# Optimization experiments

Measured on AMD Instinct MI355X. Metric: run time of the kernel, lower is better.

Reference implementation:

```python
import jax, jax.numpy as jnp
import numpy as np

B, T, D, E, H, K = 4, 4096, 1024, 8, 512, 2  # batch, seq, n_embed, num_experts, bottleneck, top_k


def setup_inputs() -> dict:
    key = jax.random.key(0)
    ks = jax.random.split(key, 8)
    s = 0.02  # param scale (original zero-inits adapters; random used for a meaningful baseline)
    return {
        "x": jax.random.normal(ks[0], (B, T, D), jnp.float32),
        "Wr": (jax.random.normal(ks[1], (D, E), jnp.float32) * s),
        "br": jnp.zeros((E,), jnp.float32),
        "Wn": (jax.random.normal(ks[2], (D, E), jnp.float32) * s),
        "bn": jnp.zeros((E,), jnp.float32),
        "Wd": (jax.random.normal(ks[3], (E, D, H), jnp.float32) * s),
        "bd": jnp.zeros((E, H), jnp.float32),
        "Wu": (jax.random.normal(ks[4], (E, H, D), jnp.float32) * s),
        "bu": jnp.zeros((E, D), jnp.float32),
        "noise": jax.random.normal(ks[5], (B, T, E), jnp.float32),
        "top_k": K,
    }


def reference(x, Wr, br, Wn, bn, Wd, bd, Wu, bu, noise, top_k):
    # --- NoisyTopkRouter ---
    logits = x @ Wr + br                                   # [B,T,E]
    noise_logits = x @ Wn + bn                             # [B,T,E]
    noisy = logits + noise * jax.nn.softplus(noise_logits)  # randn * softplus(noise_logits)
    _, idx = jax.lax.top_k(noisy, top_k)                   # [B,T,K]
    # mask of selected experts; where(mask, noisy, -inf) == scatter(top_k_logits into -inf)
    mask = jax.nn.one_hot(idx, noisy.shape[-1], dtype=jnp.bool_).any(axis=-2)  # [B,T,E]
    sparse = jnp.where(mask, noisy, -jnp.inf)
    gates = jax.nn.softmax(sparse, axis=-1)                # zeros for unselected experts

    # --- Experts (dense grouped form; gate==0 exactly kills unselected experts incl. biases) ---
    down = jnp.einsum('btd,edh->bteh', x, Wd) + bd         # [B,T,E,H]
    hidden = jax.nn.gelu(down, approximate=False)          # torch GELU is exact (erf)
    up = jnp.einsum('bteh,ehd->bted', hidden, Wu) + bu     # [B,T,E,D]
    return jnp.einsum('bted,bte->btd', up, gates)          # gate-weighted combine
```

## Files before the change

### kernel.cpp

```cpp
#include <hip/hip_runtime.h>
#include <hip/hip_bf16.h>
#include <hip/hip_fp16.h>
#include <math.h>

#define DD   1024
#define EE   8
#define HH   512
#define NTOK 16384
#define NG   16
#define MAXMT 24
#define NT   (NG * MAXMT)

typedef __attribute__((ext_vector_type(8))) short short8;
typedef __attribute__((ext_vector_type(4))) float floatx4;

__device__ __forceinline__ ushort f2bfu(float f) {
    __hip_bfloat16 h = __float2bfloat16(f);
    return *reinterpret_cast<ushort*>(&h);
}
__device__ __forceinline__ float bfu2f(ushort u) {
    union { unsigned u; float f; } cv; cv.u = ((unsigned)u) << 16; return cv.f;
}

__device__ __forceinline__ void glds16(const void* g, void* l) {
    __builtin_amdgcn_global_load_lds(
        (const __attribute__((address_space(1))) unsigned int*)g,
        (__attribute__((address_space(3))) unsigned int*)l, 16, 0, 0);
}

__global__ __launch_bounds__(256) void trans_k(const float* __restrict__ src, ushort* __restrict__ dst,
                                               const int R, const int C, int* __restrict__ cnt) {
    if (cnt && blockIdx.x == 0 && blockIdx.y == 0 && blockIdx.z == 0 && threadIdx.x < 256)
        cnt[threadIdx.x] = 0;
    const int e = blockIdx.z, r0 = blockIdx.y * 64, c0 = blockIdx.x * 64;
    __shared__ float t[64][65];
    const int tid = threadIdx.x;
    const int cseg = (tid & 15) * 4, rr = tid >> 4;
#pragma unroll
    for (int j = 0; j < 4; ++j) {
        const int r = rr + j * 16;
        const float4 v = *(const float4*)(src + ((size_t)e * R + r0 + r) * C + c0 + cseg);
        t[r][cseg] = v.x; t[r][cseg+1] = v.y; t[r][cseg+2] = v.z; t[r][cseg+3] = v.w;
    }
    __syncthreads();
    const int rseg = (tid & 15) * 4;
#pragma unroll
    for (int j = 0; j < 4; ++j) {
        const int crow = (tid >> 4) + j * 16;
        ushort o[4];
#pragma unroll
        for (int q = 0; q < 4; ++q) o[q] = f2bfu(t[rseg + q][crow]);
        *(uint2*)(dst + ((size_t)e * C + c0 + crow) * R + r0 + rseg) = *(uint2*)o;
    }
}

#define ROUTER_TAIL(AR, AN, T) do {                                           \
    const int t_ = (T);                                                       \
    float noisy[EE];                                                          \
    _Pragma("unroll")                                                         \
    for (int e = 0; e < EE; ++e) {                                            \
        const float lg = AR[e] + br[e];                                       \
        const float nl = AN[e] + bn[e];                                       \
        const float sp = fmaxf(nl, 0.f) + log1pf(expf(-fabsf(nl)));           \
        noisy[e] = lg + noise[(size_t)t_ * EE + e] * sp;                      \
    }                                                                         \
    int i0 = 0;                                                               \
    _Pragma("unroll")                                                         \
    for (int e = 1; e < EE; ++e) if (noisy[e] > noisy[i0]) i0 = e;            \
    int i1 = (i0 == 0) ? 1 : 0;                                               \
    _Pragma("unroll")                                                         \
    for (int e = 0; e < EE; ++e) if (e != i0 && noisy[e] > noisy[i1]) i1 = e; \
    const float ex = expf(noisy[i1] - noisy[i0]);                             \
    const float g0 = 1.f / (1.f + ex);                                        \
    const float g1 = ex / (1.f + ex);                                         \
    __half h0 = __float2half_rn(g0), h1 = __float2half_rn(g1);                \
    const unsigned u0 = (unsigned)t_ | ((unsigned)*reinterpret_cast<ushort*>(&h0) << 16); \
    const unsigned u1 = (unsigned)t_ | ((unsigned)*reinterpret_cast<ushort*>(&h1) << 16); \
    const int ga = i0 * 2 + 0, gb = i1 * 2 + 1;                               \
    int p0 = atomicAdd(&cnt[ga * 16], 1);                                     \
    entries[ga * NTOK + p0] = u0;                                             \
    int p1 = atomicAdd(&cnt[gb * 16], 1);                                     \
    entries[gb * NTOK + p1] = u1;                                             \
} while (0)

__global__ __launch_bounds__(512) void router_k(
    const float* __restrict__ x, const float* __restrict__ Wr, const float* __restrict__ br,
    const float* __restrict__ Wn, const float* __restrict__ bn, const float* __restrict__ noise,
    int* __restrict__ cnt, unsigned* __restrict__ entries, ushort* __restrict__ xb)
{
    __shared__ __align__(16) float WT[DD * 20];

    const int tid = threadIdx.x;
    {
        const int d0 = tid * 2;
#pragma unroll
        for (int r = 0; r < 2; ++r) {
            const int d = d0 + r;
            float4 a = *(const float4*)(Wr + (size_t)d * EE);
            float4 b = *(const float4*)(Wr + (size_t)d * EE + 4);
            float4 c = *(const float4*)(Wn + (size_t)d * EE);
            float4 e4 = *(const float4*)(Wn + (size_t)d * EE + 4);
            float* row = &WT[d * 20];
            *(float4*)(row + 0)  = a;
            *(float4*)(row + 4)  = b;
            *(float4*)(row + 8)  = c;
            *(float4*)(row + 12) = e4;
        }
    }
    __syncthreads();

    const int wave = tid >> 6;
    const int lane = tid & 63;
    const int t0 = blockIdx.x * 16 + wave * 2;

    float a0r[EE], a0n[EE], a1r[EE], a1n[EE];
#pragma unroll
    for (int e = 0; e < EE; ++e) { a0r[e] = 0.f; a0n[e] = 0.f; a1r[e] = 0.f; a1n[e] = 0.f; }

    const float* xr0 = x + (size_t)t0 * DD;
    const float* xr1 = xr0 + DD;
    ushort* xb0 = xb + (size_t)t0 * DD;
    ushort* xb1 = xb0 + DD;

#pragma unroll 4
    for (int s = 0; s < DD / 64; ++s) {
        const int d = s * 64 + lane;
        const float x0 = xr0[d];
        const float x1 = xr1[d];
        xb0[d] = f2bfu(x0);
        xb1[d] = f2bfu(x1);
        const float* row = &WT[d * 20];
        const float4 w0 = *(const float4*)(row + 0);
        const float4 w1 = *(const float4*)(row + 4);
        const float4 w2 = *(const float4*)(row + 8);
        const float4 w3 = *(const float4*)(row + 12);
        const float wr[8] = { w0.x, w0.y, w0.z, w0.w, w1.x, w1.y, w1.z, w1.w };
        const float wn[8] = { w2.x, w2.y, w2.z, w2.w, w3.x, w3.y, w3.z, w3.w };
#pragma unroll
        for (int e = 0; e < EE; ++e) {
            a0r[e] = fmaf(x0, wr[e], a0r[e]);
            a0n[e] = fmaf(x0, wn[e], a0n[e]);
            a1r[e] = fmaf(x1, wr[e], a1r[e]);
            a1n[e] = fmaf(x1, wn[e], a1n[e]);
        }
    }
#pragma unroll
    for (int off = 32; off > 0; off >>= 1) {
#pragma unroll
        for (int e = 0; e < EE; ++e) {
            a0r[e] += __shfl_xor(a0r[e], off);
            a0n[e] += __shfl_xor(a0n[e], off);
            a1r[e] += __shfl_xor(a1r[e], off);
            a1n[e] += __shfl_xor(a1n[e], off);
        }
    }
    if (lane == 0) {
        ROUTER_TAIL(a0r, a0n, t0);
        ROUTER_TAIL(a1r, a1n, t0 + 1);
    }
}


__global__ __launch_bounds__(256) void down_k(
    const ushort* __restrict__ xb, const ushort* __restrict__ WdT, const float* __restrict__ bd,
    const int* __restrict__ cnt, const unsigned* __restrict__ entries, ushort* __restrict__ hid)
{
    const int bx = blockIdx.x;
    const int n0 = (bx / NT) * 128;
    const int tmg = bx % NT;
    const int tm = tmg % MAXMT;
    const int g = tmg / MAXMT, e = g >> 1;
    const int n_g = cnt[g * 16];
    if (tm * 128 >= n_g) return;

    int og = 0;
    for (int gg = 0; gg < g; ++gg) og += cnt[gg * 16];

    __shared__ __align__(16) ushort As[2 * 128 * 64];
    __shared__ __align__(16) ushort Bs[2 * 128 * 64];
    __shared__ unsigned ecache[128];

    const int tid = threadIdx.x, lane = tid & 63, w = tid >> 6;
    const int wm = w >> 1, wn = w & 1;
    const int fr = lane & 15, fq = lane >> 4;

    if (tid < 128) {
        const int ridx = min(tm * 128 + tid, n_g - 1);
        ecache[tid] = entries[g * NTOK + ridx];
    }
    __syncthreads();

    const int lr = lane >> 3, seg = lane & 7;
    const int slog = seg ^ lr;
    const ushort* gA[4]; const ushort* gB[4];
    int loff[4];
    const ushort* WTe = WdT + (size_t)e * HH * DD;
#pragma unroll
    for (int j = 0; j < 4; ++j) {
        const int row = w * 32 + j * 8 + lr;
        const int tok = (int)(ecache[row] & 0xFFFFu);
        gA[j] = xb + (size_t)tok * DD + slog * 8;
        gB[j] = WTe + (size_t)(n0 + row) * DD + slog * 8;
        loff[j] = (w * 256 + j * 64) * 16;
    }

    floatx4 acc[4][4];
#pragma unroll
    for (int i = 0; i < 4; ++i)
#pragma unroll
        for (int j = 0; j < 4; ++j) acc[i][j] = (floatx4){0.f, 0.f, 0.f, 0.f};

    const int axr = wm * 64 + fr;
    const int bxr = wn * 64 + fr;

#pragma unroll
    for (int j = 0; j < 4; ++j) {
        glds16(gA[j], (char*)As + loff[j]);
        glds16(gB[j], (char*)Bs + loff[j]);
    }
    __syncthreads();

    int cur = 0;
    for (int k0 = 0; k0 < DD; k0 += 64) {
        if (k0 + 64 < DD) {
            const int nb = (cur ^ 1) * 16384;
#pragma unroll
            for (int j = 0; j < 4; ++j) {
                glds16(gA[j] + k0 + 64, (char*)As + nb + loff[j]);
                glds16(gB[j] + k0 + 64, (char*)Bs + nb + loff[j]);
            }
        }
        const int cb = cur * 8192;
#pragma unroll
        for (int kh = 0; kh < 2; ++kh) {
            short8 a[4], b[4];
#pragma unroll
            for (int mt = 0; mt < 4; ++mt) {
                const int r = axr + mt * 16;
                a[mt] = *(const short8*)&As[cb + r * 64 + ((kh * 4 + fq) ^ (r & 7)) * 8];
            }
#pragma unroll
            for (int nt = 0; nt < 4; ++nt) {
                const int r = bxr + nt * 16;
                b[nt] = *(const short8*)&Bs[cb + r * 64 + ((kh * 4 + fq) ^ (r & 7)) * 8];
            }
#pragma unroll
            for (int mt = 0; mt < 4; ++mt)
#pragma unroll
                for (int nt = 0; nt < 4; ++nt)
                    acc[mt][nt] = __builtin_amdgcn_mfma_f32_16x16x32_bf16(a[mt], b[nt], acc[mt][nt], 0, 0, 0);
        }
        __syncthreads();
        cur ^= 1;
    }

    const int hbase = og + tm * 128;
#pragma unroll
    for (int nt = 0; nt < 4; ++nt) {
        const int n = n0 + wn * 64 + nt * 16 + fr;
        const float bias = bd[e * HH + n];
#pragma unroll
        for (int mt = 0; mt < 4; ++mt)
#pragma unroll
            for (int i = 0; i < 4; ++i) {
                const int rl = wm * 64 + mt * 16 + fq * 4 + i;
                if (tm * 128 + rl < n_g) {
                    const float v = acc[mt][nt][i] + bias;
                    const float ge = 0.5f * v * (1.f + erff(v * 0.7071067811865475f));
                    hid[(size_t)(hbase + rl) * HH + n] = f2bfu(ge);
                }
            }
    }
}

__global__ __launch_bounds__(256) void up_k(
    const ushort* __restrict__ hid, const ushort* __restrict__ WuT, const float* __restrict__ bu,
    const int* __restrict__ cnt, const unsigned* __restrict__ entries, ushort* __restrict__ slots)
{
    const int bx = blockIdx.x;
    const int n0 = (bx / NT) * 128;
    const int tmg = bx % NT;
    const int tm = tmg % MAXMT;
    const int g = tmg / MAXMT, e = g >> 1, slot = g & 1;
    const int n_g = cnt[g * 16];
    if (tm * 128 >= n_g) return;

    int hbase = 0;
    for (int gg = 0; gg < g; ++gg) hbase += cnt[gg * 16];

    __shared__ __align__(16) ushort As[2 * 128 * 64];
    __shared__ __align__(16) ushort Bs[2 * 128 * 64];
    __shared__ unsigned ecache[128];

    const int tid = threadIdx.x, lane = tid & 63, w = tid >> 6;
    const int wm = w >> 1, wn = w & 1;
    const int fr = lane & 15, fq = lane >> 4;

    if (tid < 128) {
        const int ridx = min(tm * 128 + tid, n_g - 1);
        ecache[tid] = entries[g * NTOK + ridx];
    }
    __syncthreads();

    const int lr = lane >> 3, seg = lane & 7;
    const int slog = seg ^ lr;
    const ushort* gA[4]; const ushort* gB[4];
    int loff[4];
    const ushort* WTe = WuT + (size_t)e * DD * HH;
#pragma unroll
    for (int j = 0; j < 4; ++j) {
        const int row = w * 32 + j * 8 + lr;
        const int ar = min(tm * 128 + row, n_g - 1);
        gA[j] = hid + (size_t)(hbase + ar) * HH + slog * 8;
        gB[j] = WTe + (size_t)(n0 + row) * HH + slog * 8;
        loff[j] = (w * 256 + j * 64) * 16;
    }

    floatx4 acc[4][4];
#pragma unroll
    for (int i = 0; i < 4; ++i)
#pragma unroll
        for (int j = 0; j < 4; ++j) acc[i][j] = (floatx4){0.f, 0.f, 0.f, 0.f};

    const int axr = wm * 64 + fr;
    const int bxr = wn * 64 + fr;

#pragma unroll
    for (int j = 0; j < 4; ++j) {
        glds16(gA[j], (char*)As + loff[j]);
        glds16(gB[j], (char*)Bs + loff[j]);
    }
    __syncthreads();

    int cur = 0;
    for (int k0 = 0; k0 < HH; k0 += 64) {
        if (k0 + 64 < HH) {
            const int nb = (cur ^ 1) * 16384;
#pragma unroll
            for (int j = 0; j < 4; ++j) {
                glds16(gA[j] + k0 + 64, (char*)As + nb + loff[j]);
                glds16(gB[j] + k0 + 64, (char*)Bs + nb + loff[j]);
            }
        }
        const int cb = cur * 8192;
#pragma unroll
        for (int kh = 0; kh < 2; ++kh) {
            short8 a[4], b[4];
#pragma unroll
            for (int mt = 0; mt < 4; ++mt) {
                const int r = axr + mt * 16;
                a[mt] = *(const short8*)&As[cb + r * 64 + ((kh * 4 + fq) ^ (r & 7)) * 8];
            }
#pragma unroll
            for (int nt = 0; nt < 4; ++nt) {
                const int r = bxr + nt * 16;
                b[nt] = *(const short8*)&Bs[cb + r * 64 + ((kh * 4 + fq) ^ (r & 7)) * 8];
            }
#pragma unroll
            for (int mt = 0; mt < 4; ++mt)
#pragma unroll
                for (int nt = 0; nt < 4; ++nt)
                    acc[mt][nt] = __builtin_amdgcn_mfma_f32_16x16x32_bf16(a[mt], b[nt], acc[mt][nt], 0, 0, 0);
        }
        __syncthreads();
        cur ^= 1;
    }

#pragma unroll
    for (int nt = 0; nt < 4; ++nt) {
        const int n = n0 + wn * 64 + nt * 16 + fr;
        const float bias = bu[e * DD + n];
#pragma unroll
        for (int mt = 0; mt < 4; ++mt)
#pragma unroll
            for (int i = 0; i < 4; ++i) {
                const int rl = wm * 64 + mt * 16 + fq * 4 + i;
                if (tm * 128 + rl < n_g) {
                    const unsigned en = ecache[rl];
                    const int tok = (int)(en & 0xFFFFu);
                    ushort hb = (ushort)(en >> 16);
                    const float gate = __half2float(*reinterpret_cast<__half*>(&hb));
                    const float v = (acc[mt][nt][i] + bias) * gate;
                    slots[((size_t)tok * 2 + slot) * DD + n] = f2bfu(v);
                }
            }
    }
}

__global__ __launch_bounds__(256) void combine_k(
    const ushort* __restrict__ slots, float* __restrict__ out)
{
    const size_t flat = ((size_t)blockIdx.x * 256 + threadIdx.x) * 8;
    const size_t t = flat >> 10;
    const size_t d = flat & (DD - 1);
    union { uint4 v; ushort h[8]; } a, b;
    a.v = *(const uint4*)(slots + ((t * 2 + 0) << 10) + d);
    b.v = *(const uint4*)(slots + ((t * 2 + 1) << 10) + d);
    float o[8];
#pragma unroll
    for (int j = 0; j < 8; ++j) o[j] = bfu2f(a.h[j]) + bfu2f(b.h[j]);
    *(float4*)(out + flat) = *(const float4*)&o[0];
    *(float4*)(out + flat + 4) = *(const float4*)&o[4];
}

extern "C" void kernel_launch(void* const* d_in, const int* in_sizes, int n_in,
                              void* d_out, int out_size, void* d_ws, size_t ws_size,
                              hipStream_t stream)
{
    const float* x     = (const float*)d_in[0];
    const float* Wr    = (const float*)d_in[1];
    const float* br    = (const float*)d_in[2];
    const float* Wn    = (const float*)d_in[3];
    const float* bn    = (const float*)d_in[4];
    const float* Wd    = (const float*)d_in[5];
    const float* bd    = (const float*)d_in[6];
    const float* Wu    = (const float*)d_in[7];
    const float* bu    = (const float*)d_in[8];
    const float* noise = (const float*)d_in[9];

    char* ws = (char*)d_ws;
    int*      cnt     = (int*)(ws + 0);
    unsigned* entries = (unsigned*)(ws + 2048);
    ushort*   xb      = (ushort*)(ws + 1050624);
    ushort*   WdT     = (ushort*)(ws + 34605056);
    ushort*   WuT     = (ushort*)(ws + 42993664);
    ushort*   hid     = (ushort*)(ws + 51382272);
    ushort*   slots   = (ushort*)(ws + 84936704);

    trans_k<<<dim3(HH / 64, DD / 64, EE), 256, 0, stream>>>(Wd, WdT, DD, HH, cnt);
    trans_k<<<dim3(DD / 64, HH / 64, EE), 256, 0, stream>>>(Wu, WuT, HH, DD, nullptr);
    router_k<<<NTOK / 16, 512, 0, stream>>>(x, Wr, br, Wn, bn, noise, cnt, entries, xb);
    down_k<<<NT * 4, 256, 0, stream>>>(xb, WdT, bd, cnt, entries, hid);
    up_k<<<NT * 8, 256, 0, stream>>>(hid, WuT, bu, cnt, entries, slots);
    combine_k<<<(NTOK * DD) / (256 * 8), 256, 0, stream>>>(slots, (float*)d_out);
}
```

Before: 456.0 us.

## Merge per-slot expert groups, swizzle block order, and use finer-grained pipeline barriers

Token routing now groups by expert alone instead of by expert and slot, with the slot index packed into bit 14 of each entry. This halves the number of groups and makes each expert's M tiles larger and fewer partial. Block indices are remapped with an interleaving swizzle across workgroups. The GEMM main loops swap the full __syncthreads for an explicit vmcnt(8) wait plus a raw s_barrier, so the next stage's prefetch stays in flight, and raise wave priority around the MFMA section. The risks are a 14-bit token field, which is just enough for 16384 tokens, and the hand-written waitcnt counting being correct.

```diff
diff --git a/kernel.cpp b/kernel.cpp
--- a/kernel.cpp
+++ b/kernel.cpp
@@ -7,9 +7,11 @@
 #define EE   8
 #define HH   512
 #define NTOK 16384
-#define NG   16
-#define MAXMT 24
-#define NT   (NG * MAXMT)
+#define MAXMT 40
+#define NSL_D 4
+#define NSL_U 8
+#define NWD  (EE * MAXMT * NSL_D)
+#define NWU  (EE * MAXMT * NSL_U)
 
 typedef __attribute__((ext_vector_type(8))) short short8;
 typedef __attribute__((ext_vector_type(4))) float floatx4;
@@ -75,12 +77,11 @@
     const float g1 = ex / (1.f + ex);                                         \
     __half h0 = __float2half_rn(g0), h1 = __float2half_rn(g1);                \
     const unsigned u0 = (unsigned)t_ | ((unsigned)*reinterpret_cast<ushort*>(&h0) << 16); \
-    const unsigned u1 = (unsigned)t_ | ((unsigned)*reinterpret_cast<ushort*>(&h1) << 16); \
-    const int ga = i0 * 2 + 0, gb = i1 * 2 + 1;                               \
-    int p0 = atomicAdd(&cnt[ga * 16], 1);                                     \
-    entries[ga * NTOK + p0] = u0;                                             \
-    int p1 = atomicAdd(&cnt[gb * 16], 1);                                     \
-    entries[gb * NTOK + p1] = u1;                                             \
+    const unsigned u1 = (unsigned)t_ | (1u << 14) | ((unsigned)*reinterpret_cast<ushort*>(&h1) << 16); \
+    int p0 = atomicAdd(&cnt[i0 * 16], 1);                                     \
+    entries[i0 * NTOK + p0] = u0;                                             \
+    int p1 = atomicAdd(&cnt[i1 * 16], 1);                                     \
+    entries[i1 * NTOK + p1] = u1;                                             \
 } while (0)
 
 __global__ __launch_bounds__(512) void router_k(
@@ -166,10 +167,11 @@
     const int* __restrict__ cnt, const unsigned* __restrict__ entries, ushort* __restrict__ hid)
 {
     const int bx = blockIdx.x;
-    const int n0 = (bx / NT) * 128;
-    const int tmg = bx % NT;
-    const int tm = tmg % MAXMT;
-    const int g = tmg / MAXMT, e = g >> 1;
+    const int wid = (bx & 7) * (NWD >> 3) + (bx >> 3);
+    const int n0 = (wid % NSL_D) * 128;
+    const int tile = wid / NSL_D;
+    const int tm = tile % MAXMT;
+    const int g = tile / MAXMT, e = g;
     const int n_g = cnt[g * 16];
     if (tm * 128 >= n_g) return;
 
@@ -198,7 +200,7 @@
 #pragma unroll
     for (int j = 0; j < 4; ++j) {
         const int row = w * 32 + j * 8 + lr;
-        const int tok = (int)(ecache[row] & 0xFFFFu);
+        const int tok = (int)(ecache[row] & 0x3FFFu);
         gA[j] = xb + (size_t)tok * DD + slog * 8;
         gB[j] = WTe + (size_t)(n0 + row) * DD + slog * 8;
         loff[j] = (w * 256 + j * 64) * 16;
@@ -218,7 +220,6 @@
         glds16(gA[j], (char*)As + loff[j]);
         glds16(gB[j], (char*)Bs + loff[j]);
     }
-    __syncthreads();
 
     int cur = 0;
     for (int k0 = 0; k0 < DD; k0 += 64) {
@@ -229,8 +230,15 @@
                 glds16(gA[j] + k0 + 64, (char*)As + nb + loff[j]);
                 glds16(gB[j] + k0 + 64, (char*)Bs + nb + loff[j]);
             }
-        }
+            asm volatile("s_waitcnt vmcnt(8)" ::: "memory");
+        } else {
+            asm volatile("s_waitcnt vmcnt(0)" ::: "memory");
+        }
+        __builtin_amdgcn_sched_barrier(0);
+        __builtin_amdgcn_s_barrier();
+        asm volatile("" ::: "memory");
         const int cb = cur * 8192;
+        __builtin_amdgcn_s_setprio(1);
 #pragma unroll
         for (int kh = 0; kh < 2; ++kh) {
             short8 a[4], b[4];
@@ -250,7 +258,9 @@
                 for (int nt = 0; nt < 4; ++nt)
                     acc[mt][nt] = __builtin_amdgcn_mfma_f32_16x16x32_bf16(a[mt], b[nt], acc[mt][nt], 0, 0, 0);
         }
-        __syncthreads();
+        __builtin_amdgcn_s_setprio(0);
+        asm volatile("" ::: "memory");
+        __builtin_amdgcn_s_barrier();
         cur ^= 1;
     }
 
@@ -278,10 +288,11 @@
     const int* __restrict__ cnt, const unsigned* __restrict__ entries, ushort* __restrict__ slots)
 {
     const int bx = blockIdx.x;
-    const int n0 = (bx / NT) * 128;
-    const int tmg = bx % NT;
-    const int tm = tmg % MAXMT;
-    const int g = tmg / MAXMT, e = g >> 1, slot = g & 1;
+    const int wid = (bx & 7) * (NWU >> 3) + (bx >> 3);
+    const int n0 = (wid % NSL_U) * 128;
+    const int tile = wid / NSL_U;
+    const int tm = tile % MAXMT;
+    const int g = tile / MAXMT, e = g;
     const int n_g = cnt[g * 16];
     if (tm * 128 >= n_g) return;
 
@@ -330,7 +341,6 @@
         glds16(gA[j], (char*)As + loff[j]);
         glds16(gB[j], (char*)Bs + loff[j]);
     }
-    __syncthreads();
 
     int cur = 0;
     for (int k0 = 0; k0 < HH; k0 += 64) {
@@ -341,8 +351,15 @@
                 glds16(gA[j] + k0 + 64, (char*)As + nb + loff[j]);
                 glds16(gB[j] + k0 + 64, (char*)Bs + nb + loff[j]);
             }
-        }
+            asm volatile("s_waitcnt vmcnt(8)" ::: "memory");
+        } else {
+            asm volatile("s_waitcnt vmcnt(0)" ::: "memory");
+        }
+        __builtin_amdgcn_sched_barrier(0);
+        __builtin_amdgcn_s_barrier();
+        asm volatile("" ::: "memory");
         const int cb = cur * 8192;
+        __builtin_amdgcn_s_setprio(1);
 #pragma unroll
         for (int kh = 0; kh < 2; ++kh) {
             short8 a[4], b[4];
@@ -362,7 +379,9 @@
                 for (int nt = 0; nt < 4; ++nt)
                     acc[mt][nt] = __builtin_amdgcn_mfma_f32_16x16x32_bf16(a[mt], b[nt], acc[mt][nt], 0, 0, 0);
         }
-        __syncthreads();
+        __builtin_amdgcn_s_setprio(0);
+        asm volatile("" ::: "memory");
+        __builtin_amdgcn_s_barrier();
         cur ^= 1;
     }
 
@@ -377,7 +396,8 @@
                 const int rl = wm * 64 + mt * 16 + fq * 4 + i;
                 if (tm * 128 + rl < n_g) {
                     const unsigned en = ecache[rl];
-                    const int tok = (int)(en & 0xFFFFu);
+                    const int tok = (int)(en & 0x3FFFu);
+                    const int slot = (int)((en >> 14) & 1u);
                     ushort hb = (ushort)(en >> 16);
                     const float gate = __half2float(*reinterpret_cast<__half*>(&hb));
                     const float v = (acc[mt][nt][i] + bias) * gate;
@@ -430,7 +450,7 @@
     trans_k<<<dim3(HH / 64, DD / 64, EE), 256, 0, stream>>>(Wd, WdT, DD, HH, cnt);
     trans_k<<<dim3(DD / 64, HH / 64, EE), 256, 0, stream>>>(Wu, WuT, HH, DD, nullptr);
     router_k<<<NTOK / 16, 512, 0, stream>>>(x, Wr, br, Wn, bn, noise, cnt, entries, xb);
-    down_k<<<NT * 4, 256, 0, stream>>>(xb, WdT, bd, cnt, entries, hid);
-    up_k<<<NT * 8, 256, 0, stream>>>(hid, WuT, bu, cnt, entries, slots);
+    down_k<<<NWD, 256, 0, stream>>>(xb, WdT, bd, cnt, entries, hid);
+    up_k<<<NWU, 256, 0, stream>>>(hid, WuT, bu, cnt, entries, slots);
     combine_k<<<(NTOK * DD) / (256 * 8), 256, 0, stream>>>(slots, (float*)d_out);
 }
```

New measurement: 447.4 us. About the same (-1.9%).
